# Kernel optimization log

Hardware: AMD Instinct MI355X
Metric: run time of the kernel (lower is better)

Reference implementation:

```python
import jax, jax.numpy as jnp
import numpy as np

B, S, D, N, H, K = 32, 512, 2048, 16, 128, 64
EPS = 1e-6


def setup_inputs() -> dict:
    key = jax.random.key(0)
    ks = jax.random.split(key, 8)
    # glorot-uniform-like scale for the (D, N, H) attention kernels
    kern_scale = (6.0 / (D + H)) ** 0.5
    down_sd = 1.0 / K  # matches module: mean 0, sd = 1/downsampling_k
    q = jax.random.normal(ks[0], (B, S, D), dtype=jnp.float32)
    k = jax.random.normal(ks[1], (B, S, D), dtype=jnp.float32)
    v = jax.random.normal(ks[2], (B, S, D), dtype=jnp.float32)
    query_kernel = jax.random.uniform(ks[3], (D, N, H), jnp.float32, -kern_scale, kern_scale)
    key_kernel = jax.random.uniform(ks[4], (D, N, H), jnp.float32, -kern_scale, kern_scale)
    value_kernel = jax.random.uniform(ks[5], (D, N, H), jnp.float32, -kern_scale, kern_scale)
    key_down = down_sd * jax.random.normal(ks[6], (K, S), dtype=jnp.float32)
    value_down = down_sd * jax.random.normal(ks[7], (K, S), dtype=jnp.float32)
    return dict(q=q, k=k, v=v, query_kernel=query_kernel, key_kernel=key_kernel,
                value_kernel=value_kernel, key_down=key_down, value_down=value_down)


def reference(q, k, v, query_kernel, key_kernel, value_kernel, key_down, value_down):
    # Linformer-style downsampling of keys/values along the sequence axis: [B,S,D] -> [B,K,D]
    key_ds = jnp.einsum('ks,bsd->bkd', key_down, k)
    val_ds = jnp.einsum('ks,bsd->bkd', value_down, v)
    # Per-head projections
    queries = jnp.einsum('bqd,dnh->bqnh', q, query_kernel)   # [B,S,N,H]
    keys = jnp.einsum('bkd,dnh->bknh', key_ds, key_kernel)   # [B,K,N,H]
    values = jnp.einsum('bkd,dnh->bknh', val_ds, value_kernel)  # [B,K,N,H]
    # Kernelized linear attention with elu+1 feature map (mask=False branch)
    phi_q = jax.nn.elu(queries) + 1.0
    phi_k = jax.nn.elu(keys) + 1.0
    s = jnp.einsum('bknd,bknh->bndh', phi_k, values)  # [B,N,H,H]
    z = jnp.sum(phi_k, axis=1)                        # [B,N,H]
    qs = jnp.einsum('bqnd,bndh->bqnh', phi_q, s)      # [B,S,N,H]
    qz = jnp.einsum('bqnd,bnd->bqn', phi_q, z) + EPS  # [B,S,N]
    a_v = qs / qz[..., None]
    return a_v.reshape(B, S, N * H)
```

## Files before the change

kernel.cpp:

```cpp
#include <hip/hip_runtime.h>
#include <cstdint>
#include <cstddef>

typedef float f32x4 __attribute__((ext_vector_type(4)));
typedef short s16x8 __attribute__((ext_vector_type(8)));
typedef unsigned short u16;

#define EPS 1e-6f

__device__ __forceinline__ u16 f2bf(float f) {
    unsigned u = __float_as_uint(f);
    u += 0x7FFFu + ((u >> 16) & 1u);
    return (u16)(u >> 16);
}
__device__ __forceinline__ float bf2f(u16 u) {
    return __uint_as_float(((unsigned)u) << 16);
}

typedef const __attribute__((address_space(1))) void cg_void;
typedef __attribute__((address_space(3))) void l_void;
__device__ __forceinline__ void async16(void* dst_lds, const void* src_g) {
    __builtin_amdgcn_global_load_lds((cg_void*)src_g, (l_void*)dst_lds, 16, 0, 0);
}

#define BARRIER() do { asm volatile("" ::: "memory"); \
                       __builtin_amdgcn_s_barrier();  \
                       asm volatile("" ::: "memory"); } while (0)

__global__ __launch_bounds__(256) void prep_down(
    const float* __restrict__ q, u16* __restrict__ qb,
    const float* __restrict__ w0, const float* __restrict__ w1,
    const float* __restrict__ w2, u16* __restrict__ o0,
    u16* __restrict__ o1, u16* __restrict__ o2,
    const float* __restrict__ kin, const float* __restrict__ vin,
    const float* __restrict__ wdk, const float* __restrict__ wdv,
    u16* __restrict__ kds, u16* __restrict__ vds)
{
    __shared__ __align__(16) char smem[14336];
    const int bid = blockIdx.x;
    const int tid = threadIdx.x;

    if (bid < 1024) {
        u16* At = (u16*)smem;
        u16* Bt = (u16*)(smem + 4096);
        const int sel = bid >> 9, rem = bid & 511;
        const int b = rem >> 4, d0 = (rem & 15) << 7;
        const float* x  = sel ? vin : kin;
        const float* wd = sel ? wdv : wdk;
        u16* outp       = sel ? vds : kds;
        const int w = tid >> 6, l = tid & 63, l16 = l & 15, k8 = l >> 4;
        f32x4 acc[4][2] = {};
        for (int s0 = 0; s0 < 512; s0 += 32) {
            __syncthreads();
            for (int c = tid; c < 512; c += 256) {
                int kkr = c >> 3, sc = (c & 7) << 2;
                float4 f = *(const float4*)&wd[kkr * 512 + s0 + sc];
                u16* dst = &At[kkr * 32 + sc];
                dst[0] = f2bf(f.x); dst[1] = f2bf(f.y); dst[2] = f2bf(f.z); dst[3] = f2bf(f.w);
            }
            for (int c = tid; c < 512; c += 256) {
                int sp = c >> 5, dq = (c & 31) << 2;
                int srow = sp << 1;
                const float* xp = &x[((size_t)(b * 512) + s0 + srow) * 2048 + d0 + dq];
                float4 f0 = *(const float4*)xp;
                float4 f1 = *(const float4*)(xp + 2048);
                int col = srow ^ ((c & 3) << 3);
                unsigned p0 = (unsigned)f2bf(f0.x) | ((unsigned)f2bf(f1.x) << 16);
                unsigned p1 = (unsigned)f2bf(f0.y) | ((unsigned)f2bf(f1.y) << 16);
                unsigned p2 = (unsigned)f2bf(f0.z) | ((unsigned)f2bf(f1.z) << 16);
                unsigned p3 = (unsigned)f2bf(f0.w) | ((unsigned)f2bf(f1.w) << 16);
                *(unsigned*)&Bt[(dq + 0) * 40 + col] = p0;
                *(unsigned*)&Bt[(dq + 1) * 40 + col] = p1;
                *(unsigned*)&Bt[(dq + 2) * 40 + col] = p2;
                *(unsigned*)&Bt[(dq + 3) * 40 + col] = p3;
            }
            __syncthreads();
            s16x8 af[4], bfr[2];
            #pragma unroll
            for (int fm = 0; fm < 4; ++fm)
                af[fm] = *(const s16x8*)&At[(fm * 16 + l16) * 32 + k8 * 8];
            #pragma unroll
            for (int fn = 0; fn < 2; ++fn)
                bfr[fn] = *(const s16x8*)&Bt[(w * 32 + fn * 16 + l16) * 40
                                             + ((k8 ^ (l16 >> 2)) << 3)];
            #pragma unroll
            for (int fm = 0; fm < 4; ++fm)
                #pragma unroll
                for (int fn = 0; fn < 2; ++fn)
                    acc[fm][fn] = __builtin_amdgcn_mfma_f32_16x16x32_bf16(af[fm], bfr[fn], acc[fm][fn], 0, 0, 0);
        }
        #pragma unroll
        for (int fm = 0; fm < 4; ++fm)
            #pragma unroll
            for (int fn = 0; fn < 2; ++fn)
                #pragma unroll
                for (int j = 0; j < 4; ++j) {
                    int r = fm * 16 + k8 * 4 + j;
                    int c = w * 32 + fn * 16 + l16;
                    outp[((size_t)(b * 64 + r)) * 2048 + d0 + c] = f2bf(acc[fm][fn][j]);
                }
    } else if (bid < 4096) {
        u16* tl = (u16*)smem;
        int wb = bid - 1024;
        int which = wb >> 10;
        int t = wb & 1023;
        const float* in = which == 0 ? w0 : which == 1 ? w1 : w2;
        u16* out        = which == 0 ? o0 : which == 1 ? o1 : o2;
        int bx = (t & 31) * 64, by = (t >> 5) * 64;
        int tx = tid & 63, ty = tid >> 6;
        #pragma unroll 4
        for (int i = ty; i < 64; i += 4)
            tl[tx * 68 + i] = f2bf(in[(size_t)(by + i) * 2048 + bx + tx]);
        __syncthreads();
        int srow = tid >> 2, sq = tid & 3;
        const u16* lp = &tl[srow * 68 + sq * 16];
        u16* op = &out[(size_t)(bx + srow) * 2048 + by + sq * 16];
        #pragma unroll
        for (int j8 = 0; j8 < 4; ++j8)
            *(short4*)(op + j8 * 4) = *(const short4*)(lp + j8 * 4);
    } else {
        int cb = bid - 4096;
        size_t base = (size_t)cb * 256 + tid;
        #pragma unroll
        for (int it = 0; it < 8; ++it) {
            size_t i = base + (size_t)it * 1048576;
            float4 f = ((const float4*)q)[i];
            ushort4 o;
            o.x = f2bf(f.x); o.y = f2bf(f.y); o.z = f2bf(f.z); o.w = f2bf(f.w);
            ((ushort4*)qb)[i] = o;
        }
    }
}

__global__ __launch_bounds__(512, 2) void gemm256_elu(
    const u16* __restrict__ A, const u16* __restrict__ BT,
    u16* __restrict__ C, int M, int N, int K)
{
    __shared__ __align__(16) u16 lds[8][8192];
    const int tid = threadIdx.x;
    const int w = tid >> 6, l = tid & 63;
    const int wm = w >> 2, wn = w & 3;
    const int l16 = l & 15, k8 = l >> 4;
    const int NT = K >> 6;

    const int nbn = N >> 8;
    const int nwg = gridDim.x;
    int wg = blockIdx.x;
    if ((nwg & 7) == 0) wg = (wg & 7) * (nwg >> 3) + (wg >> 3);
    const int row0 = (wg / nbn) << 8, col0 = (wg % nbn) << 8;

    const int lr  = l >> 3;
    const int scb = (((l & 7) ^ lr) << 4);
    const int swzr = (l16 & 7) << 4;

#define PANEL(s, m, h) (&lds[((s) << 2) | ((m) << 1) | (h)][0])

#define STG(pan, G, prow0, kk0) do {                                             \
        _Pragma("unroll")                                                        \
        for (int i_ = 0; i_ < 2; ++i_) {                                         \
            int seg_ = w + (i_ << 3);                                            \
            const u16* src_ = (G) + (size_t)((prow0) + (seg_ << 3) + lr) * K     \
                              + (kk0) + (scb >> 1);                              \
            async16((pan) + (seg_ << 9), src_);                                  \
        } } while (0)

#define LDA(slot, mh) do { const u16* p_ = PANEL(slot, 0, mh);                   \
        _Pragma("unroll")                                                        \
        for (int fm_ = 0; fm_ < 4; ++fm_)                                        \
        _Pragma("unroll")                                                        \
        for (int ks_ = 0; ks_ < 2; ++ks_)                                        \
            Af[fm_][ks_] = *(const s16x8*)(p_ + (wm * 64 + fm_ * 16 + l16) * 64  \
                           + (((ks_ * 64 + k8 * 16) ^ swzr) >> 1)); } while (0)

#define LDB(slot, nh, dst) do { const u16* p_ = PANEL(slot, 1, nh);              \
        _Pragma("unroll")                                                        \
        for (int fn_ = 0; fn_ < 2; ++fn_)                                        \
        _Pragma("unroll")                                                        \
        for (int ks_ = 0; ks_ < 2; ++ks_)                                        \
            dst[fn_][ks_] = *(const s16x8*)(p_ + (wn * 32 + fn_ * 16 + l16) * 64 \
                           + (((ks_ * 64 + k8 * 16) ^ swzr) >> 1)); } while (0)

#define MM(mh, nh, BF) do {                                                      \
        __builtin_amdgcn_s_setprio(1);                                           \
        _Pragma("unroll")                                                        \
        for (int fm_ = 0; fm_ < 4; ++fm_)                                        \
        _Pragma("unroll")                                                        \
        for (int fn_ = 0; fn_ < 2; ++fn_)                                        \
        _Pragma("unroll")                                                        \
        for (int ks_ = 0; ks_ < 2; ++ks_)                                        \
            acc[mh][nh][fm_][fn_] = __builtin_amdgcn_mfma_f32_16x16x32_bf16(     \
                Af[fm_][ks_], BF[fn_][ks_], acc[mh][nh][fm_][fn_], 0, 0, 0);     \
        __builtin_amdgcn_s_setprio(0); } while (0)

#define TILE(t, cur, nxt, BFc, BFn) do {                                         \
        LDA(cur, 0);                                                             \
        if ((t) + 1 < NT) STG(PANEL(nxt, 0, 1), A, row0 + 128, ((t) + 1) << 6);  \
        BARRIER(); MM(0, 0, BFc); BARRIER();                                     \
        LDB(cur, 1, Bf1);                                                        \
        if ((t) + 2 < NT) STG(PANEL(cur, 0, 0), A, row0, ((t) + 2) << 6);        \
        BARRIER(); MM(0, 1, Bf1); BARRIER();                                     \
        LDA(cur, 1);                                                             \
        if ((t) + 2 < NT) STG(PANEL(cur, 1, 0), BT, col0, ((t) + 2) << 6);       \
        BARRIER(); MM(1, 1, Bf1); BARRIER();                                     \
        if ((t) + 2 < NT) STG(PANEL(cur, 1, 1), BT, col0 + 128, ((t) + 2) << 6); \
        BARRIER(); MM(1, 0, BFc);                                                \
        if ((t) == NT - 2)     asm volatile("s_waitcnt vmcnt(0)" ::: "memory");  \
        else if ((t) < NT - 2) asm volatile("s_waitcnt vmcnt(6)" ::: "memory");  \
        BARRIER();                                                               \
        if ((t) + 1 < NT) LDB(nxt, 0, BFn);                                      \
    } while (0)

    f32x4 acc[2][2][4][2] = {};
    s16x8 Af[4][2], Bf0a[2][2], Bf0b[2][2], Bf1[2][2];

    STG(PANEL(0, 0, 0), A,  row0,       0);
    STG(PANEL(0, 1, 0), BT, col0,       0);
    STG(PANEL(0, 1, 1), BT, col0 + 128, 0);
    STG(PANEL(0, 0, 1), A,  row0 + 128, 0);
    STG(PANEL(1, 0, 0), A,  row0,       64);
    STG(PANEL(1, 1, 0), BT, col0,       64);
    STG(PANEL(1, 1, 1), BT, col0 + 128, 64);
    asm volatile("s_waitcnt vmcnt(6)" ::: "memory");
    BARRIER();
    LDB(0, 0, Bf0a);

    for (int t = 0; t < NT; t += 2) {
        TILE(t,     0, 1, Bf0a, Bf0b);
        TILE(t + 1, 1, 0, Bf0b, Bf0a);
    }
#undef PANEL
#undef STG
#undef LDA
#undef LDB
#undef MM
#undef TILE

    #pragma unroll
    for (int mh = 0; mh < 2; ++mh)
        #pragma unroll
        for (int fm = 0; fm < 4; ++fm)
            #pragma unroll
            for (int j = 0; j < 4; ++j) {
                int r = row0 + mh * 128 + wm * 64 + fm * 16 + k8 * 4 + j;
                size_t rb = (size_t)r * N;
                #pragma unroll
                for (int nh = 0; nh < 2; ++nh)
                    #pragma unroll
                    for (int fn = 0; fn < 2; ++fn) {
                        int c = col0 + nh * 128 + wn * 32 + fn * 16 + l16;
                        float x = acc[mh][nh][fm][fn][j];
                        x = x > 0.0f ? x + 1.0f : __expf(x);
                        C[rb + c] = f2bf(x);
                    }
            }
}

__global__ __launch_bounds__(256) void gemm128_dual(
    const u16* __restrict__ A0, const u16* __restrict__ B0, u16* __restrict__ C0,
    const u16* __restrict__ A1, const u16* __restrict__ B1, u16* __restrict__ C1)
{
    const u16* A  = blockIdx.z ? A1 : A0;
    const u16* BT = blockIdx.z ? B1 : B0;
    u16* C        = blockIdx.z ? C1 : C0;
    const bool elu = (blockIdx.z == 0);
    const int K = 2048;

    __shared__ __align__(16) u16 lds[2][8192];
    const int tid = threadIdx.x;
    const int w = tid >> 6, l = tid & 63;
    const int wm = w >> 1, wn = w & 1;
    const int l16 = l & 15, k8 = l >> 4;
    const int sr = (w << 4) + (l >> 2);
    const int sc = (l & 3) << 3;
    const int row0 = blockIdx.y * 128, col0 = blockIdx.x * 128;
    const int nk = K >> 5;
    f32x4 acc[4][4] = {};

#define STAGE(buf, kt) do {                                                        \
        int kk0 = (kt) << 5;                                                       \
        _Pragma("unroll")                                                          \
        for (int i = 0; i < 2; ++i) {                                              \
            const u16* ga = A + (size_t)(row0 + i * 64 + sr) * K + kk0 + sc;       \
            async16(&lds[buf][i * 2048 + (w << 9)], ga);                           \
            const u16* gb = BT + (size_t)(col0 + i * 64 + sr) * K + kk0 + sc;      \
            async16(&lds[buf][4096 + i * 2048 + (w << 9)], gb);                    \
        }                                                                          \
    } while (0)

    STAGE(0, 0);
    asm volatile("s_waitcnt vmcnt(0)" ::: "memory");
    __syncthreads();
    int cur = 0;
    for (int kt = 0; kt < nk; ++kt) {
        if (kt + 1 < nk) STAGE(cur ^ 1, kt + 1);
        s16x8 af[4], bfr[4];
        const u16* Ab = &lds[cur][0];
        const u16* Bb = &lds[cur][4096];
        #pragma unroll
        for (int fm = 0; fm < 4; ++fm)
            af[fm] = *(const s16x8*)&Ab[((wm << 6) + (fm << 4) + l16) * 32 + (k8 << 3)];
        #pragma unroll
        for (int fn = 0; fn < 4; ++fn)
            bfr[fn] = *(const s16x8*)&Bb[((wn << 6) + (fn << 4) + l16) * 32 + (k8 << 3)];
        #pragma unroll
        for (int fm = 0; fm < 4; ++fm)
            #pragma unroll
            for (int fn = 0; fn < 4; ++fn)
                acc[fm][fn] = __builtin_amdgcn_mfma_f32_16x16x32_bf16(af[fm], bfr[fn], acc[fm][fn], 0, 0, 0);
        __syncthreads();
        cur ^= 1;
    }
#undef STAGE

    #pragma unroll
    for (int fm = 0; fm < 4; ++fm)
        #pragma unroll
        for (int j = 0; j < 4; ++j) {
            int r = row0 + (wm << 6) + (fm << 4) + (k8 << 2) + j;
            size_t rbase = (size_t)r * 2048;
            #pragma unroll
            for (int fn = 0; fn < 4; ++fn) {
                int c = col0 + (wn << 6) + (fn << 4) + l16;
                float x = acc[fm][fn][j];
                if (elu) x = x > 0.0f ? x + 1.0f : __expf(x);
                C[rbase + c] = f2bf(x);
            }
        }
}

__global__ __launch_bounds__(256) void sz_kernel(
    const u16* __restrict__ phik, const u16* __restrict__ vals,
    u16* __restrict__ sT, float* __restrict__ z)
{
    int b = blockIdx.x >> 4, n = blockIdx.x & 15;
    __shared__ __align__(16) u16 pk[64 * 128];
    __shared__ __align__(16) u16 vv[64 * 128];
    int tid = threadIdx.x;
    for (int i = tid; i < 1024; i += 256) {
        int r = i >> 4, c8 = (i & 15) << 3;
        size_t g = ((size_t)(b * 64 + r)) * 2048 + n * 128 + c8;
        ((s16x8*)pk)[i] = *(const s16x8*)&phik[g];
        ((s16x8*)vv)[i] = *(const s16x8*)&vals[g];
    }
    __syncthreads();
    if (tid < 128) {
        float s = 0.0f;
        for (int kk = 0; kk < 64; ++kk) s += bf2f(pk[kk * 128 + tid]);
        z[((size_t)(b * 16 + n)) * 128 + tid] = s;
    }
    int hg = tid >> 4, dg = tid & 15;
    int h0 = hg * 8, d0 = dg * 8;
    float acc[8][8] = {};
    for (int kk = 0; kk < 64; ++kk) {
        s16x8 vr = *(const s16x8*)&vv[kk * 128 + h0];
        s16x8 pr = *(const s16x8*)&pk[kk * 128 + d0];
        float va[8], pa[8];
        #pragma unroll
        for (int i = 0; i < 8; ++i) { va[i] = bf2f((u16)vr[i]); pa[i] = bf2f((u16)pr[i]); }
        #pragma unroll
        for (int i = 0; i < 8; ++i)
            #pragma unroll
            for (int j = 0; j < 8; ++j)
                acc[i][j] += va[i] * pa[j];
    }
    size_t base = ((size_t)(b * 16 + n)) * 16384;
    #pragma unroll
    for (int i = 0; i < 8; ++i) {
        u16 row[8];
        #pragma unroll
        for (int j = 0; j < 8; ++j) row[j] = f2bf(acc[i][j]);
        *(s16x8*)&sT[base + (size_t)(h0 + i) * 128 + d0] = *(s16x8*)row;
    }
}

__global__ __launch_bounds__(256) void qs_kernel(
    const u16* __restrict__ phiq, const u16* __restrict__ sT,
    const float* __restrict__ z, float* __restrict__ out)
{
    const int gb = blockIdx.x;
    const int rb = gb & 3, bn = gb >> 2;
    const int b = bn >> 4, n = bn & 15;
    __shared__ __align__(16) u16 Blds[128 * 128];
    const int tid = threadIdx.x;
    const int w = tid >> 6, l = tid & 63;
    const int l16 = l & 15, k8 = l >> 4;

    {
        const u16* base = sT + (size_t)bn * 16384;
        #pragma unroll
        for (int r0 = 0; r0 < 128; r0 += 16) {
            int row = r0 + (w << 2) + (l >> 4);
            int scb = (((l & 15) ^ (row & 7)) << 4);
            async16(&Blds[(r0 + (w << 2)) * 128], base + (size_t)row * 128 + (scb >> 1));
        }
    }

    const size_t arow0 = (size_t)(b * 512 + rb * 128);
    s16x8 Af[2][4];
    #pragma unroll
    for (int fm = 0; fm < 2; ++fm)
        #pragma unroll
        for (int ks = 0; ks < 4; ++ks) {
            int row = (w << 5) + (fm << 4) + l16;
            Af[fm][ks] = *(const s16x8*)(phiq + (arow0 + row) * 2048 + n * 128
                                         + (ks << 5) + (k8 << 3));
        }

    s16x8 Bz[4];
    #pragma unroll
    for (int ks = 0; ks < 4; ++ks) {
        const float* zp = z + (size_t)bn * 128 + (ks << 5) + (k8 << 3);
        float4 f0 = *(const float4*)zp;
        float4 f1 = *(const float4*)(zp + 4);
        u16 tmp[8] = { f2bf(f0.x), f2bf(f0.y), f2bf(f0.z), f2bf(f0.w),
                       f2bf(f1.x), f2bf(f1.y), f2bf(f1.z), f2bf(f1.w) };
        Bz[ks] = *(const s16x8*)tmp;
    }

    f32x4 accz[2] = {};
    #pragma unroll
    for (int fm = 0; fm < 2; ++fm)
        #pragma unroll
        for (int ks = 0; ks < 4; ++ks)
            accz[fm] = __builtin_amdgcn_mfma_f32_16x16x32_bf16(Af[fm][ks], Bz[ks], accz[fm], 0, 0, 0);

    asm volatile("s_waitcnt vmcnt(0)" ::: "memory");
    BARRIER();

    const int swz = (l16 & 7) << 4;
    f32x4 acc[2][8] = {};
    #pragma unroll
    for (int fn = 0; fn < 8; ++fn) {
        s16x8 Bf[4];
        #pragma unroll
        for (int ks = 0; ks < 4; ++ks)
            Bf[ks] = *(const s16x8*)&Blds[((fn << 4) + l16) * 128
                                          + ((((ks << 6) + (k8 << 4)) ^ swz) >> 1)];
        #pragma unroll
        for (int fm = 0; fm < 2; ++fm)
            #pragma unroll
            for (int ks = 0; ks < 4; ++ks)
                acc[fm][fn] = __builtin_amdgcn_mfma_f32_16x16x32_bf16(Af[fm][ks], Bf[ks], acc[fm][fn], 0, 0, 0);
    }

    #pragma unroll
    for (int fm = 0; fm < 2; ++fm)
        #pragma unroll
        for (int j = 0; j < 4; ++j) {
            int row = (w << 5) + (fm << 4) + (k8 << 2) + j;
            float rq = 1.0f / (accz[fm][j] + EPS);
            size_t ob = (arow0 + row) * 2048 + n * 128;
            #pragma unroll
            for (int fn = 0; fn < 8; ++fn)
                out[ob + (fn << 4) + l16] = acc[fm][fn][j] * rq;
        }
}

extern "C" void kernel_launch(void* const* d_in, const int* in_sizes, int n_in,
                              void* d_out, int out_size, void* d_ws, size_t ws_size,
                              hipStream_t stream) {
    (void)in_sizes; (void)n_in; (void)out_size; (void)ws_size;
    const float* q   = (const float*)d_in[0];
    const float* k   = (const float*)d_in[1];
    const float* v   = (const float*)d_in[2];
    const float* wq  = (const float*)d_in[3];
    const float* wk  = (const float*)d_in[4];
    const float* wv  = (const float*)d_in[5];
    const float* kdw = (const float*)d_in[6];
    const float* vdw = (const float*)d_in[7];
    float* out = (float*)d_out;

    char* p = (char*)d_ws;
    u16* qb   = (u16*)p; p += (size_t)16384 * 2048 * 2;
    u16* wqT  = (u16*)p; p += (size_t)2048 * 2048 * 2;
    u16* wkT  = (u16*)p; p += (size_t)2048 * 2048 * 2;
    u16* wvT  = (u16*)p; p += (size_t)2048 * 2048 * 2;
    u16* kds  = (u16*)p; p += (size_t)2048 * 2048 * 2;
    u16* vds  = (u16*)p; p += (size_t)2048 * 2048 * 2;
    u16* phiq = (u16*)p; p += (size_t)16384 * 2048 * 2;
    u16* phik = (u16*)p; p += (size_t)2048 * 2048 * 2;
    u16* vals = (u16*)p; p += (size_t)2048 * 2048 * 2;
    u16* sT   = (u16*)p; p += (size_t)512 * 128 * 128 * 2;
    float* z  = (float*)p; p += (size_t)512 * 128 * 4;

    prep_down<<<8192, 256, 0, stream>>>(q, qb, wq, wk, wv, wqT, wkT, wvT,
                                        k, v, kdw, vdw, kds, vds);
    gemm128_dual<<<dim3(16, 16, 2), 256, 0, stream>>>(kds, wkT, phik, vds, wvT, vals);
    gemm256_elu<<<512, 512, 0, stream>>>(qb, wqT, phiq, 16384, 2048, 2048);
    sz_kernel<<<512, 256, 0, stream>>>(phik, vals, sT, z);
    qs_kernel<<<2048, 256, 0, stream>>>(phiq, sT, z, out);
}
```

Before: 380.5 us.

## Fuse s/z computation into qs kernel and split prep kernel into cast and downsample

Merges sz_kernel into the final qs kernel, so each (batch, head) block computes phi_k^T V and z in shared memory and then loops over all four row blocks of queries. This removes the sT/z round trip through global memory and one launch. It also cuts the parallel grid for the final stage from 2048 to 512 blocks and raises shared-memory use per block, which may lower occupancy. The downsampling MFMA work is moved out of the prep kernel into its own launch, so the cast blocks no longer carry the larger LDS footprint.

```diff
diff --git a/kernel.cpp b/kernel.cpp
--- a/kernel.cpp
+++ b/kernel.cpp
@@ -27,83 +27,18 @@
                        __builtin_amdgcn_s_barrier();  \
                        asm volatile("" ::: "memory"); } while (0)
 
-__global__ __launch_bounds__(256) void prep_down(
+__global__ __launch_bounds__(256) void prep_cast(
     const float* __restrict__ q, u16* __restrict__ qb,
     const float* __restrict__ w0, const float* __restrict__ w1,
     const float* __restrict__ w2, u16* __restrict__ o0,
-    u16* __restrict__ o1, u16* __restrict__ o2,
-    const float* __restrict__ kin, const float* __restrict__ vin,
-    const float* __restrict__ wdk, const float* __restrict__ wdv,
-    u16* __restrict__ kds, u16* __restrict__ vds)
+    u16* __restrict__ o1, u16* __restrict__ o2)
 {
-    __shared__ __align__(16) char smem[14336];
+    __shared__ u16 tl[64 * 68];
     const int bid = blockIdx.x;
     const int tid = threadIdx.x;
-
-    if (bid < 1024) {
-        u16* At = (u16*)smem;
-        u16* Bt = (u16*)(smem + 4096);
-        const int sel = bid >> 9, rem = bid & 511;
-        const int b = rem >> 4, d0 = (rem & 15) << 7;
-        const float* x  = sel ? vin : kin;
-        const float* wd = sel ? wdv : wdk;
-        u16* outp       = sel ? vds : kds;
-        const int w = tid >> 6, l = tid & 63, l16 = l & 15, k8 = l >> 4;
-        f32x4 acc[4][2] = {};
-        for (int s0 = 0; s0 < 512; s0 += 32) {
-            __syncthreads();
-            for (int c = tid; c < 512; c += 256) {
-                int kkr = c >> 3, sc = (c & 7) << 2;
-                float4 f = *(const float4*)&wd[kkr * 512 + s0 + sc];
-                u16* dst = &At[kkr * 32 + sc];
-                dst[0] = f2bf(f.x); dst[1] = f2bf(f.y); dst[2] = f2bf(f.z); dst[3] = f2bf(f.w);
-            }
-            for (int c = tid; c < 512; c += 256) {
-                int sp = c >> 5, dq = (c & 31) << 2;
-                int srow = sp << 1;
-                const float* xp = &x[((size_t)(b * 512) + s0 + srow) * 2048 + d0 + dq];
-                float4 f0 = *(const float4*)xp;
-                float4 f1 = *(const float4*)(xp + 2048);
-                int col = srow ^ ((c & 3) << 3);
-                unsigned p0 = (unsigned)f2bf(f0.x) | ((unsigned)f2bf(f1.x) << 16);
-                unsigned p1 = (unsigned)f2bf(f0.y) | ((unsigned)f2bf(f1.y) << 16);
-                unsigned p2 = (unsigned)f2bf(f0.z) | ((unsigned)f2bf(f1.z) << 16);
-                unsigned p3 = (unsigned)f2bf(f0.w) | ((unsigned)f2bf(f1.w) << 16);
-                *(unsigned*)&Bt[(dq + 0) * 40 + col] = p0;
-                *(unsigned*)&Bt[(dq + 1) * 40 + col] = p1;
-                *(unsigned*)&Bt[(dq + 2) * 40 + col] = p2;
-                *(unsigned*)&Bt[(dq + 3) * 40 + col] = p3;
-            }
-            __syncthreads();
-            s16x8 af[4], bfr[2];
-            #pragma unroll
-            for (int fm = 0; fm < 4; ++fm)
-                af[fm] = *(const s16x8*)&At[(fm * 16 + l16) * 32 + k8 * 8];
-            #pragma unroll
-            for (int fn = 0; fn < 2; ++fn)
-                bfr[fn] = *(const s16x8*)&Bt[(w * 32 + fn * 16 + l16) * 40
-                                             + ((k8 ^ (l16 >> 2)) << 3)];
-            #pragma unroll
-            for (int fm = 0; fm < 4; ++fm)
-                #pragma unroll
-                for (int fn = 0; fn < 2; ++fn)
-                    acc[fm][fn] = __builtin_amdgcn_mfma_f32_16x16x32_bf16(af[fm], bfr[fn], acc[fm][fn], 0, 0, 0);
-        }
-        #pragma unroll
-        for (int fm = 0; fm < 4; ++fm)
-            #pragma unroll
-            for (int fn = 0; fn < 2; ++fn)
-                #pragma unroll
-                for (int j = 0; j < 4; ++j) {
-                    int r = fm * 16 + k8 * 4 + j;
-                    int c = w * 32 + fn * 16 + l16;
-                    outp[((size_t)(b * 64 + r)) * 2048 + d0 + c] = f2bf(acc[fm][fn][j]);
-                }
-    } else if (bid < 4096) {
-        u16* tl = (u16*)smem;
-        int wb = bid - 1024;
-        int which = wb >> 10;
-        int t = wb & 1023;
+    if (bid < 3072) {
+        int which = bid >> 10;
+        int t = bid & 1023;
         const float* in = which == 0 ? w0 : which == 1 ? w1 : w2;
         u16* out        = which == 0 ? o0 : which == 1 ? o1 : o2;
         int bx = (t & 31) * 64, by = (t >> 5) * 64;
@@ -119,7 +54,7 @@
         for (int j8 = 0; j8 < 4; ++j8)
             *(short4*)(op + j8 * 4) = *(const short4*)(lp + j8 * 4);
     } else {
-        int cb = bid - 4096;
+        int cb = bid - 3072;
         size_t base = (size_t)cb * 256 + tid;
         #pragma unroll
         for (int it = 0; it < 8; ++it) {
@@ -130,6 +65,73 @@
             ((ushort4*)qb)[i] = o;
         }
     }
+}
+
+__global__ __launch_bounds__(256) void down_mfma(
+    const float* __restrict__ kin, const float* __restrict__ vin,
+    const float* __restrict__ wdk, const float* __restrict__ wdv,
+    u16* __restrict__ kds, u16* __restrict__ vds)
+{
+    __shared__ __align__(16) u16 At[64 * 32];
+    __shared__ __align__(16) u16 Bt[128 * 40];
+    const int bid = blockIdx.x;
+    const int tid = threadIdx.x;
+    const int sel = bid >> 9, rem = bid & 511;
+    const int b = rem >> 4, d0 = (rem & 15) << 7;
+    const float* x  = sel ? vin : kin;
+    const float* wd = sel ? wdv : wdk;
+    u16* outp       = sel ? vds : kds;
+    const int w = tid >> 6, l = tid & 63, l16 = l & 15, k8 = l >> 4;
+    f32x4 acc[4][2] = {};
+    for (int s0 = 0; s0 < 512; s0 += 32) {
+        __syncthreads();
+        for (int c = tid; c < 512; c += 256) {
+            int kkr = c >> 3, sc = (c & 7) << 2;
+            float4 f = *(const float4*)&wd[kkr * 512 + s0 + sc];
+            u16* dst = &At[kkr * 32 + sc];
+            dst[0] = f2bf(f.x); dst[1] = f2bf(f.y); dst[2] = f2bf(f.z); dst[3] = f2bf(f.w);
+        }
+        for (int c = tid; c < 512; c += 256) {
+            int sp = c >> 5, dq = (c & 31) << 2;
+            int srow = sp << 1;
+            const float* xp = &x[((size_t)(b * 512) + s0 + srow) * 2048 + d0 + dq];
+            float4 f0 = *(const float4*)xp;
+            float4 f1 = *(const float4*)(xp + 2048);
+            int col = srow ^ ((c & 3) << 3);
+            unsigned p0 = (unsigned)f2bf(f0.x) | ((unsigned)f2bf(f1.x) << 16);
+            unsigned p1 = (unsigned)f2bf(f0.y) | ((unsigned)f2bf(f1.y) << 16);
+            unsigned p2 = (unsigned)f2bf(f0.z) | ((unsigned)f2bf(f1.z) << 16);
+            unsigned p3 = (unsigned)f2bf(f0.w) | ((unsigned)f2bf(f1.w) << 16);
+            *(unsigned*)&Bt[(dq + 0) * 40 + col] = p0;
+            *(unsigned*)&Bt[(dq + 1) * 40 + col] = p1;
+            *(unsigned*)&Bt[(dq + 2) * 40 + col] = p2;
+            *(unsigned*)&Bt[(dq + 3) * 40 + col] = p3;
+        }
+        __syncthreads();
+        s16x8 af[4], bfr[2];
+        #pragma unroll
+        for (int fm = 0; fm < 4; ++fm)
+            af[fm] = *(const s16x8*)&At[(fm * 16 + l16) * 32 + k8 * 8];
+        #pragma unroll
+        for (int fn = 0; fn < 2; ++fn)
+            bfr[fn] = *(const s16x8*)&Bt[(w * 32 + fn * 16 + l16) * 40
+                                         + ((k8 ^ (l16 >> 2)) << 3)];
+        #pragma unroll
+        for (int fm = 0; fm < 4; ++fm)
+            #pragma unroll
+            for (int fn = 0; fn < 2; ++fn)
+                acc[fm][fn] = __builtin_amdgcn_mfma_f32_16x16x32_bf16(af[fm], bfr[fn], acc[fm][fn], 0, 0, 0);
+    }
+    #pragma unroll
+    for (int fm = 0; fm < 4; ++fm)
+        #pragma unroll
+        for (int fn = 0; fn < 2; ++fn)
+            #pragma unroll
+            for (int j = 0; j < 4; ++j) {
+                int r = fm * 16 + k8 * 4 + j;
+                int c = w * 32 + fn * 16 + l16;
+                outp[((size_t)(b * 64 + r)) * 2048 + d0 + c] = f2bf(acc[fm][fn][j]);
+            }
 }
 
 __global__ __launch_bounds__(512, 2) void gemm256_elu(
@@ -328,88 +330,66 @@
         }
 }
 
-__global__ __launch_bounds__(256) void sz_kernel(
-    const u16* __restrict__ phik, const u16* __restrict__ vals,
-    u16* __restrict__ sT, float* __restrict__ z)
+__global__ __launch_bounds__(256) void qs_fused(
+    const u16* __restrict__ phiq, const u16* __restrict__ phik,
+    const u16* __restrict__ vals, float* __restrict__ out)
 {
-    int b = blockIdx.x >> 4, n = blockIdx.x & 15;
     __shared__ __align__(16) u16 pk[64 * 128];
     __shared__ __align__(16) u16 vv[64 * 128];
-    int tid = threadIdx.x;
-    for (int i = tid; i < 1024; i += 256) {
-        int r = i >> 4, c8 = (i & 15) << 3;
-        size_t g = ((size_t)(b * 64 + r)) * 2048 + n * 128 + c8;
-        ((s16x8*)pk)[i] = *(const s16x8*)&phik[g];
-        ((s16x8*)vv)[i] = *(const s16x8*)&vals[g];
-    }
-    __syncthreads();
-    if (tid < 128) {
-        float s = 0.0f;
-        for (int kk = 0; kk < 64; ++kk) s += bf2f(pk[kk * 128 + tid]);
-        z[((size_t)(b * 16 + n)) * 128 + tid] = s;
-    }
-    int hg = tid >> 4, dg = tid & 15;
-    int h0 = hg * 8, d0 = dg * 8;
-    float acc[8][8] = {};
-    for (int kk = 0; kk < 64; ++kk) {
-        s16x8 vr = *(const s16x8*)&vv[kk * 128 + h0];
-        s16x8 pr = *(const s16x8*)&pk[kk * 128 + d0];
-        float va[8], pa[8];
-        #pragma unroll
-        for (int i = 0; i < 8; ++i) { va[i] = bf2f((u16)vr[i]); pa[i] = bf2f((u16)pr[i]); }
-        #pragma unroll
-        for (int i = 0; i < 8; ++i)
-            #pragma unroll
-            for (int j = 0; j < 8; ++j)
-                acc[i][j] += va[i] * pa[j];
-    }
-    size_t base = ((size_t)(b * 16 + n)) * 16384;
-    #pragma unroll
-    for (int i = 0; i < 8; ++i) {
-        u16 row[8];
-        #pragma unroll
-        for (int j = 0; j < 8; ++j) row[j] = f2bf(acc[i][j]);
-        *(s16x8*)&sT[base + (size_t)(h0 + i) * 128 + d0] = *(s16x8*)row;
-    }
-}
-
-__global__ __launch_bounds__(256) void qs_kernel(
-    const u16* __restrict__ phiq, const u16* __restrict__ sT,
-    const float* __restrict__ z, float* __restrict__ out)
-{
-    const int gb = blockIdx.x;
-    const int rb = gb & 3, bn = gb >> 2;
+    __shared__ __align__(16) u16 Blds[128 * 128];
+    __shared__ float zl[128];
+    const int bn = blockIdx.x;
     const int b = bn >> 4, n = bn & 15;
-    __shared__ __align__(16) u16 Blds[128 * 128];
     const int tid = threadIdx.x;
     const int w = tid >> 6, l = tid & 63;
     const int l16 = l & 15, k8 = l >> 4;
 
+    for (int i = tid; i < 1024; i += 256) {
+        size_t g = ((size_t)(b * 64 + (i >> 4))) * 2048 + n * 128 + ((i & 15) << 3);
+        async16(&pk[i << 3], &phik[g]);
+        async16(&vv[i << 3], &vals[g]);
+    }
+    asm volatile("s_waitcnt vmcnt(0)" ::: "memory");
+    __syncthreads();
+
     {
-        const u16* base = sT + (size_t)bn * 16384;
-        #pragma unroll
-        for (int r0 = 0; r0 < 128; r0 += 16) {
-            int row = r0 + (w << 2) + (l >> 4);
-            int scb = (((l & 15) ^ (row & 7)) << 4);
-            async16(&Blds[(r0 + (w << 2)) * 128], base + (size_t)row * 128 + (scb >> 1));
-        }
-    }
-
-    const size_t arow0 = (size_t)(b * 512 + rb * 128);
-    s16x8 Af[2][4];
-    #pragma unroll
-    for (int fm = 0; fm < 2; ++fm)
-        #pragma unroll
-        for (int ks = 0; ks < 4; ++ks) {
-            int row = (w << 5) + (fm << 4) + l16;
-            Af[fm][ks] = *(const s16x8*)(phiq + (arow0 + row) * 2048 + n * 128
-                                         + (ks << 5) + (k8 << 3));
-        }
-
+        int hg = tid >> 4, dg = tid & 15;
+        int h0 = hg * 8, d0 = dg * 8;
+        float acc[8][8] = {};
+        for (int kk = 0; kk < 64; ++kk) {
+            s16x8 vr = *(const s16x8*)&vv[kk * 128 + h0];
+            s16x8 pr = *(const s16x8*)&pk[kk * 128 + d0];
+            float va[8], pa[8];
+            #pragma unroll
+            for (int i = 0; i < 8; ++i) { va[i] = bf2f((u16)vr[i]); pa[i] = bf2f((u16)pr[i]); }
+            #pragma unroll
+            for (int i = 0; i < 8; ++i)
+                #pragma unroll
+                for (int j = 0; j < 8; ++j)
+                    acc[i][j] += va[i] * pa[j];
+        }
+        if (tid < 128) {
+            float s = 0.0f;
+            for (int kk = 0; kk < 64; ++kk) s += bf2f(pk[kk * 128 + tid]);
+            zl[tid] = s;
+        }
+        #pragma unroll
+        for (int i = 0; i < 8; ++i) {
+            int row = h0 + i;
+            u16 rowv[8];
+            #pragma unroll
+            for (int j = 0; j < 8; ++j) rowv[j] = f2bf(acc[i][j]);
+            int boff = (dg << 4) ^ ((row & 7) << 4);
+            *(s16x8*)&Blds[row * 128 + (boff >> 1)] = *(s16x8*)rowv;
+        }
+    }
+    __syncthreads();
+
+    const int swz = (l16 & 7) << 4;
     s16x8 Bz[4];
     #pragma unroll
     for (int ks = 0; ks < 4; ++ks) {
-        const float* zp = z + (size_t)bn * 128 + (ks << 5) + (k8 << 3);
+        const float* zp = &zl[(ks << 5) + (k8 << 3)];
         float4 f0 = *(const float4*)zp;
         float4 f1 = *(const float4*)(zp + 4);
         u16 tmp[8] = { f2bf(f0.x), f2bf(f0.y), f2bf(f0.z), f2bf(f0.w),
@@ -417,43 +397,51 @@
         Bz[ks] = *(const s16x8*)tmp;
     }
 
-    f32x4 accz[2] = {};
-    #pragma unroll
-    for (int fm = 0; fm < 2; ++fm)
-        #pragma unroll
-        for (int ks = 0; ks < 4; ++ks)
-            accz[fm] = __builtin_amdgcn_mfma_f32_16x16x32_bf16(Af[fm][ks], Bz[ks], accz[fm], 0, 0, 0);
-
-    asm volatile("s_waitcnt vmcnt(0)" ::: "memory");
-    BARRIER();
-
-    const int swz = (l16 & 7) << 4;
-    f32x4 acc[2][8] = {};
-    #pragma unroll
-    for (int fn = 0; fn < 8; ++fn) {
-        s16x8 Bf[4];
-        #pragma unroll
-        for (int ks = 0; ks < 4; ++ks)
-            Bf[ks] = *(const s16x8*)&Blds[((fn << 4) + l16) * 128
-                                          + ((((ks << 6) + (k8 << 4)) ^ swz) >> 1)];
+    for (int rb = 0; rb < 4; ++rb) {
+        const size_t arow0 = (size_t)(b * 512 + rb * 128);
+        s16x8 Af[2][4];
         #pragma unroll
         for (int fm = 0; fm < 2; ++fm)
             #pragma unroll
+            for (int ks = 0; ks < 4; ++ks) {
+                int row = (w << 5) + (fm << 4) + l16;
+                Af[fm][ks] = *(const s16x8*)(phiq + (arow0 + row) * 2048 + n * 128
+                                             + (ks << 5) + (k8 << 3));
+            }
+        f32x4 accz[2] = {};
+        #pragma unroll
+        for (int fm = 0; fm < 2; ++fm)
+            #pragma unroll
             for (int ks = 0; ks < 4; ++ks)
-                acc[fm][fn] = __builtin_amdgcn_mfma_f32_16x16x32_bf16(Af[fm][ks], Bf[ks], acc[fm][fn], 0, 0, 0);
-    }
-
-    #pragma unroll
-    for (int fm = 0; fm < 2; ++fm)
-        #pragma unroll
-        for (int j = 0; j < 4; ++j) {
-            int row = (w << 5) + (fm << 4) + (k8 << 2) + j;
-            float rq = 1.0f / (accz[fm][j] + EPS);
-            size_t ob = (arow0 + row) * 2048 + n * 128;
-            #pragma unroll
-            for (int fn = 0; fn < 8; ++fn)
-                out[ob + (fn << 4) + l16] = acc[fm][fn][j] * rq;
-        }
+                accz[fm] = __builtin_amdgcn_mfma_f32_16x16x32_bf16(Af[fm][ks], Bz[ks], accz[fm], 0, 0, 0);
+
+        f32x4 acc2[2][8] = {};
+        #pragma unroll
+        for (int fn = 0; fn < 8; ++fn) {
+            s16x8 Bfr[4];
+            #pragma unroll
+            for (int ks = 0; ks < 4; ++ks)
+                Bfr[ks] = *(const s16x8*)&Blds[((fn << 4) + l16) * 128
+                                               + ((((ks << 6) + (k8 << 4)) ^ swz) >> 1)];
+            #pragma unroll
+            for (int fm = 0; fm < 2; ++fm)
+                #pragma unroll
+                for (int ks = 0; ks < 4; ++ks)
+                    acc2[fm][fn] = __builtin_amdgcn_mfma_f32_16x16x32_bf16(Af[fm][ks], Bfr[ks], acc2[fm][fn], 0, 0, 0);
+        }
+
+        #pragma unroll
+        for (int fm = 0; fm < 2; ++fm)
+            #pragma unroll
+            for (int j = 0; j < 4; ++j) {
+                int row = (w << 5) + (fm << 4) + (k8 << 2) + j;
+                float rq = 1.0f / (accz[fm][j] + EPS);
+                size_t ob = (arow0 + row) * 2048 + n * 128;
+                #pragma unroll
+                for (int fn = 0; fn < 8; ++fn)
+                    out[ob + (fn << 4) + l16] = acc2[fm][fn][j] * rq;
+            }
+    }
 }
 
 extern "C" void kernel_launch(void* const* d_in, const int* in_sizes, int n_in,
@@ -480,13 +468,10 @@
     u16* phiq = (u16*)p; p += (size_t)16384 * 2048 * 2;
     u16* phik = (u16*)p; p += (size_t)2048 * 2048 * 2;
     u16* vals = (u16*)p; p += (size_t)2048 * 2048 * 2;
-    u16* sT   = (u16*)p; p += (size_t)512 * 128 * 128 * 2;
-    float* z  = (float*)p; p += (size_t)512 * 128 * 4;
-
-    prep_down<<<8192, 256, 0, stream>>>(q, qb, wq, wk, wv, wqT, wkT, wvT,
-                                        k, v, kdw, vdw, kds, vds);
+
+    prep_cast<<<7168, 256, 0, stream>>>(q, qb, wq, wk, wv, wqT, wkT, wvT);
+    down_mfma<<<1024, 256, 0, stream>>>(k, v, kdw, vdw, kds, vds);
     gemm128_dual<<<dim3(16, 16, 2), 256, 0, stream>>>(kds, wkT, phik, vds, wvT, vals);
     gemm256_elu<<<512, 512, 0, stream>>>(qb, wqT, phiq, 16384, 2048, 2048);
-    sz_kernel<<<512, 256, 0, stream>>>(phik, vals, sT, z);
-    qs_kernel<<<2048, 256, 0, stream>>>(phiq, sT, z, out);
-}
+    qs_fused<<<512, 256, 0, stream>>>(phiq, phik, vals, out);
+}
```

After: 374.1 us. Within noise of the previous version (-1.7%).
